# Performance work log

Measured on AMD Instinct MI355X. Metric: run time of the kernel, lower is better.

## Reference

```python
import jax, jax.numpy as jnp
import numpy as np

D = 512
H = 8
DH = D // H  # 64


def setup_inputs() -> dict:
    key = jax.random.key(0)
    ks = jax.random.split(key, 7)
    batch, la, lb = 8, 256, 256
    A = jax.random.normal(ks[0], (batch, la, D), dtype=jnp.float32)
    B = jax.random.normal(ks[1], (batch, lb, D), dtype=jnp.float32)
    s = 1.0 / np.sqrt(D)
    W1 = jax.random.uniform(ks[2], (D, D), minval=-s, maxval=s, dtype=jnp.float32)
    b1 = jax.random.uniform(ks[3], (D,), minval=-s, maxval=s, dtype=jnp.float32)
    W2 = jax.random.uniform(ks[4], (D, D), minval=-s, maxval=s, dtype=jnp.float32)
    b2 = jax.random.uniform(ks[5], (D,), minval=-s, maxval=s, dtype=jnp.float32)
    q = jax.random.normal(ks[6], (DH,), dtype=jnp.float32) * 0.1
    return {"A": A, "B": B, "W1": W1, "b1": b1, "W2": W2, "b2": b2, "q": q}


def reference(A, B, W1, b1, W2, b2, q):
    bs, la, _ = A.shape
    lb = B.shape[1]
    # Linear + ReLU, then raw row-major reshape to (batch, heads, len, dh)
    # (matches torch .view semantics: NOT a head-transpose split)
    A_ = jax.nn.relu(A @ W1.T + b1).reshape(bs, H, la, DH)
    B_ = jax.nn.relu(B @ W2.T + b2).reshape(bs, H, lb, DH)
    # bilinear score: tanh of elementwise pairwise product, dotted with q
    # att_maps: [bs, H, la, lb]
    att_maps = jnp.einsum(
        "bhijc,c->bhij",
        jnp.tanh(A_[:, :, :, None, :] * B_[:, :, None, :, :]),
        q,
    )
    temp_b2a = jax.nn.softmax(jnp.mean(att_maps, axis=3), axis=2)  # [bs,H,la]
    temp_a2b = jax.nn.softmax(jnp.mean(att_maps, axis=2), axis=2)  # [bs,H,lb]
    A_heads = A.reshape(bs, H, la, DH)
    B_heads = B.reshape(bs, H, lb, DH)
    A_p = jnp.sum(A_heads * temp_b2a[..., None], axis=2).reshape(bs, -1)  # [bs, d]
    B_p = jnp.sum(B_heads * temp_a2b[..., None], axis=2).reshape(bs, -1)  # [bs, d]
    return (
        jnp.concatenate((A_p, B_p), axis=1),
        jnp.mean(temp_b2a, axis=1),
        jnp.mean(temp_a2b, axis=1),
    )
```

## Files before the change

kernel.cpp:

```cpp
#include <hip/hip_runtime.h>
#include <hip/hip_bf16.h>

#define LOG2E 1.4426950408889634f
#define SC2   2.8853900817779268f

typedef __attribute__((ext_vector_type(8))) short short8b;
typedef __attribute__((ext_vector_type(4))) short short4b;
typedef __attribute__((ext_vector_type(4))) float f32x4;

__device__ __forceinline__ float fast_exp2(float x) {
#if __has_builtin(__builtin_amdgcn_exp2f)
  return __builtin_amdgcn_exp2f(x);
#else
  return exp2f(x);
#endif
}
__device__ __forceinline__ float fast_rcp(float x) {
#if __has_builtin(__builtin_amdgcn_rcpf)
  return __builtin_amdgcn_rcpf(x);
#else
  return 1.0f / x;
#endif
}
__device__ __forceinline__ short f2bf(float f) {
  __hip_bfloat16 h = __float2bfloat16(f);
  return *reinterpret_cast<short*>(&h);
}

__global__ __launch_bounds__(256) void gemm_fused_kernel(
    const float* __restrict__ Xa, const float* __restrict__ Wa,
    const float* __restrict__ ba, float* __restrict__ Oa,
    const float* __restrict__ Xb, const float* __restrict__ Wb,
    const float* __restrict__ bb, const float* __restrict__ q,
    float2* __restrict__ Cb, unsigned* __restrict__ Cnt,
    float* __restrict__ Ksum) {
  const int isB = blockIdx.z;
  const float* X = isB ? Xb : Xa;
  const float* W = isB ? Wb : Wa;
  const float* bias = isB ? bb : ba;

  __shared__ __align__(16) short As[64 * 40];
  __shared__ __align__(16) short Ws[64 * 40];
  __shared__ __align__(16) float Btile[64][65];
  __shared__ float qls[64];

  int t = threadIdx.x;
  int m0 = blockIdx.x * 64, n0 = blockIdx.y * 64;
  int l = t & 63, w = t >> 6;
  int wm = (w >> 1) * 32, wn = (w & 1) * 32;
  int lr = l & 15, ko = (l >> 4) * 8;

  if (isB && t < 64) qls[t] = q[t];

  f32x4 acc[2][2];
#pragma unroll
  for (int m = 0; m < 2; ++m)
#pragma unroll
    for (int n = 0; n < 2; ++n) acc[m][n] = f32x4{0.f, 0.f, 0.f, 0.f};

  for (int k0 = 0; k0 < 512; k0 += 32) {
#pragma unroll
    for (int s = 0; s < 2; ++s) {
      int slot = t + s * 256;
      int row = slot >> 3, qd = (slot & 7) << 2;
      float4 v = *reinterpret_cast<const float4*>(&X[(m0 + row) * 512 + k0 + qd]);
      short4b sv = {f2bf(v.x), f2bf(v.y), f2bf(v.z), f2bf(v.w)};
      *reinterpret_cast<short4b*>(&As[row * 40 + qd]) = sv;
      float4 u = *reinterpret_cast<const float4*>(&W[(n0 + row) * 512 + k0 + qd]);
      short4b su = {f2bf(u.x), f2bf(u.y), f2bf(u.z), f2bf(u.w)};
      *reinterpret_cast<short4b*>(&Ws[row * 40 + qd]) = su;
    }
    __syncthreads();

    short8b afr[2], bfr[2];
#pragma unroll
    for (int m = 0; m < 2; ++m)
      afr[m] = *reinterpret_cast<const short8b*>(&As[(wm + m * 16 + lr) * 40 + ko]);
#pragma unroll
    for (int n = 0; n < 2; ++n)
      bfr[n] = *reinterpret_cast<const short8b*>(&Ws[(wn + n * 16 + lr) * 40 + ko]);
#pragma unroll
    for (int m = 0; m < 2; ++m)
#pragma unroll
      for (int n = 0; n < 2; ++n)
        acc[m][n] = __builtin_amdgcn_mfma_f32_16x16x32_bf16(afr[m], bfr[n], acc[m][n], 0, 0, 0);
    __syncthreads();
  }

  if (!isB) {
#pragma unroll
    for (int n = 0; n < 2; ++n) {
      int col = n0 + wn + n * 16 + lr;
      float bv = bias[col];
#pragma unroll
      for (int m = 0; m < 2; ++m) {
        int rbase = m0 + wm + m * 16 + (l >> 4) * 4;
#pragma unroll
        for (int r = 0; r < 4; ++r) {
          float v = acc[m][n][r] + bv;
          Oa[(rbase + r) * 512 + col] = v > 0.f ? v : 0.f;
        }
      }
    }
    return;
  }

#pragma unroll
  for (int n = 0; n < 2; ++n) {
    int col = wn + n * 16 + lr;
    float bv = bias[n0 + col];
#pragma unroll
    for (int m = 0; m < 2; ++m) {
      int rbase = wm + m * 16 + (l >> 4) * 4;
#pragma unroll
      for (int r = 0; r < 4; ++r) {
        float v = acc[m][n][r] + bv;
        Btile[rbase + r][col] = v > 0.f ? v : 0.f;
      }
    }
  }
  __syncthreads();

  int jl = t >> 2, p = t & 3;
  int row = m0 + jl;
  int bh = (row >> 8) * 8 + ((row >> 5) & 7);
  int j = ((row & 31) << 3) + (n0 >> 6);
  int c0 = p * 16;

  int nz = 0;
  float K = 0.f;
#pragma unroll
  for (int cc = 0; cc < 16; ++cc) {
    float v = Btile[jl][c0 + cc];
    if (v > 0.f) { ++nz; K += qls[c0 + cc]; }
  }
  int incl = nz;
#pragma unroll
  for (int d = 1; d < 4; d <<= 1) {
    int u = __shfl_up(incl, d, 4);
    if (p >= d) incl += u;
  }
  int off = incl - nz;
  int total = __shfl(incl, 3, 4);

  float2* dst = Cb + (bh * 256 + j) * 64;
  int k = off;
#pragma unroll
  for (int cc = 0; cc < 16; ++cc) {
    int c = c0 + cc;
    float v = Btile[jl][c];
    if (v > 0.f) {
      unsigned qb = (__float_as_uint(-2.f * qls[c]) & ~63u) | (unsigned)c;
      dst[k] = make_float2(v * SC2, __uint_as_float(qb));
      ++k;
    }
  }
  K += __shfl_xor(K, 1, 4);
  K += __shfl_xor(K, 2, 4);
  if (p == 3) {
    int cnt = total;
    while (cnt & 3) { dst[cnt] = make_float2(0.f, 0.f); ++cnt; }
    Cnt[bh * 256 + j] = (unsigned)cnt;
    Ksum[bh * 256 + j] = K;
  }
}

__global__ __launch_bounds__(512, 8) void attmap_kernel(
    const float* __restrict__ Ar, const float2* __restrict__ Cb,
    const unsigned* __restrict__ Cnt,
    float* __restrict__ rowpart, float* __restrict__ colsum) {
  int bh = blockIdx.x, jblk = blockIdx.y, isplit = blockIdx.z;
  int t = threadIdx.x;
  int il = t & 127;
  int g = __builtin_amdgcn_readfirstlane(t >> 7);
  __shared__ __align__(16) float Als[128 * 65];
  __shared__ float red[512];
  __shared__ float cpart[8][8];

  const float* Abase = Ar + bh * 16384 + isplit * 8192;
#pragma unroll
  for (int it = 0; it < 4; ++it) {
    int idx = it * 512 + t;
    int r = idx >> 4, c4 = (idx & 15) << 2;
    float4 v = *reinterpret_cast<const float4*>(&Abase[r * 64 + c4]);
    Als[r * 65 + c4 + 0] = v.x; Als[r * 65 + c4 + 1] = v.y;
    Als[r * 65 + c4 + 2] = v.z; Als[r * 65 + c4 + 3] = v.w;
  }
  __syncthreads();

  const float* Arow = &Als[il * 65];
  float acc[8];

#pragma unroll
  for (int jj = 0; jj < 8; ++jj) {
    int jl = g * 8 + jj;
    int n = (int)__builtin_amdgcn_readfirstlane(Cnt[bh * 256 + jblk * 32 + jl]);
    const float4* P4 = reinterpret_cast<const float4*>(Cb + (bh * 256 + jblk * 32 + jl) * 64);
    float s0 = 0.f, s1 = 0.f;
    if (n > 0) {
      const int nit = n >> 2;
      float4 u0 = P4[0], v0 = P4[1];
      int i1 = (1 < nit) ? 1 : (nit - 1);
      float4 u1 = P4[i1 * 2], v1 = P4[i1 * 2 + 1];
#pragma unroll 1
      for (int it = 0; it < nit; ++it) {
        int i2 = it + 2; i2 = (i2 < nit) ? i2 : (nit - 1);
        float4 u2 = P4[i2 * 2], v2 = P4[i2 * 2 + 1];
        float g0 = Arow[__float_as_uint(u0.y) & 63u];
        float g1 = Arow[__float_as_uint(u0.w) & 63u];
        float g2 = Arow[__float_as_uint(v0.y) & 63u];
        float g3 = Arow[__float_as_uint(v0.w) & 63u];
        float e0 = fast_exp2(g0 * u0.x);
        float e1 = fast_exp2(g1 * u0.z);
        float e2 = fast_exp2(g2 * v0.x);
        float e3 = fast_exp2(g3 * v0.z);
        float w0 = e0 + 1.f, w1 = e1 + 1.f, w2 = e2 + 1.f, w3 = e3 + 1.f;
        float n01 = fmaf(u0.w, w0, u0.y * w1);
        float n23 = fmaf(v0.w, w2, v0.y * w3);
        s0 = fmaf(n01, fast_rcp(w0 * w1), s0);
        s1 = fmaf(n23, fast_rcp(w2 * w3), s1);
        u0 = u1; v0 = v1; u1 = u2; v1 = v2;
      }
    }
    acc[jj] = s0 + s1;
  }

  float rs = 0.f;
#pragma unroll
  for (int jj = 0; jj < 8; ++jj) rs += acc[jj];
  red[t] = rs;

  int lane = t & 63, w = t >> 6;
#pragma unroll
  for (int jj = 0; jj < 8; ++jj) {
    float v = acc[jj];
#pragma unroll
    for (int off = 32; off >= 1; off >>= 1) v += __shfl_xor(v, off);
    if (lane == 0) cpart[w][jj] = v;
  }
  __syncthreads();
  if (t < 128) {
    rowpart[(bh * 8 + jblk) * 256 + isplit * 128 + t] =
        red[t] + red[t + 128] + red[t + 256] + red[t + 384];
  } else if (t < 160) {
    int jl = t - 128;
    int gg = jl >> 3, jj = jl & 7;
    colsum[(bh * 2 + isplit) * 256 + jblk * 32 + jl] =
        cpart[2 * gg][jj] + cpart[2 * gg + 1][jj];
  }
}

__global__ __launch_bounds__(512) void softmax_pool_kernel(
    const float* __restrict__ rowpart, const float* __restrict__ colsum,
    const float* __restrict__ Ksum,
    const float* __restrict__ A0, const float* __restrict__ B0,
    float* __restrict__ b2a, float* __restrict__ a2b,
    float* __restrict__ poolA, float* __restrict__ poolB) {
  int bh = blockIdx.x, chunk = blockIdx.y;
  int b = bh >> 3, h = bh & 7;
  int t = threadIdx.x;
  int tt = t & 255;
  int lane = t & 63, w = (t >> 6) & 3;
  __shared__ float redA[4], redB[4], redC[4], redD[4];
  __shared__ float tA[256], tB[256];
  __shared__ float pp[8][64];

  float r = 0.f;
#pragma unroll
  for (int jb = 0; jb < 8; ++jb) r += rowpart[(bh * 8 + jb) * 256 + tt];
  r *= (1.f / 256.f);
  float cs = Ksum[bh * 256 + tt] +
             (colsum[(bh * 2 + 0) * 256 + tt] + colsum[(bh * 2 + 1) * 256 + tt]) * (1.f / 256.f);

  float mr = r, mc = cs;
#pragma unroll
  for (int off = 32; off >= 1; off >>= 1) {
    mr = fmaxf(mr, __shfl_xor(mr, off));
    mc = fmaxf(mc, __shfl_xor(mc, off));
  }
  if (lane == 0) { redA[w] = mr; redB[w] = mc; }
  __syncthreads();
  mr = fmaxf(fmaxf(redA[0], redA[1]), fmaxf(redA[2], redA[3]));
  mc = fmaxf(fmaxf(redB[0], redB[1]), fmaxf(redB[2], redB[3]));

  float er = fast_exp2((r - mr) * LOG2E);
  float ec = fast_exp2((cs - mc) * LOG2E);
  float sr = er, sc = ec;
#pragma unroll
  for (int off = 32; off >= 1; off >>= 1) {
    sr += __shfl_xor(sr, off);
    sc += __shfl_xor(sc, off);
  }
  if (lane == 0) { redC[w] = sr; redD[w] = sc; }
  __syncthreads();
  sr = redC[0] + redC[1] + redC[2] + redC[3];
  sc = redD[0] + redD[1] + redD[2] + redD[3];

  float vb2a = er * fast_rcp(sr);
  float va2b = ec * fast_rcp(sc);
  tA[tt] = vb2a; tB[tt] = va2b;
  if (chunk == 0) {
    b2a[bh * 256 + tt] = vb2a;
    a2b[bh * 256 + tt] = va2b;
  }
  __syncthreads();

  int c = t & 63, isub = t >> 6;
  const float* Ab = A0 + b * 131072 + h * 16384;
  const float* Bb = B0 + b * 131072 + h * 16384;
  float pa = 0.f, pb = 0.f;
#pragma unroll
  for (int ii = 0; ii < 8; ++ii) {
    int i = chunk * 64 + isub * 8 + ii;
    pa = fmaf(Ab[i * 64 + c], tA[i], pa);
    pb = fmaf(Bb[i * 64 + c], tB[i], pb);
  }
  pp[isub][c] = pa;
  __syncthreads();
  if (t < 64) {
    float s = 0.f;
#pragma unroll
    for (int k = 0; k < 8; ++k) s += pp[k][t];
    poolA[(bh * 4 + chunk) * 64 + t] = s;
  }
  __syncthreads();
  pp[isub][c] = pb;
  __syncthreads();
  if (t < 64) {
    float s = 0.f;
#pragma unroll
    for (int k = 0; k < 8; ++k) s += pp[k][t];
    poolB[(bh * 4 + chunk) * 64 + t] = s;
  }
}

__global__ __launch_bounds__(256) void final_kernel(
    const float* __restrict__ poolA, const float* __restrict__ poolB,
    const float* __restrict__ b2a, const float* __restrict__ a2b,
    float* __restrict__ out) {
  int b = blockIdx.x, t = threadIdx.x;
  float s1 = 0.f, s2 = 0.f;
#pragma unroll
  for (int h = 0; h < 8; ++h) {
    s1 += b2a[(b * 8 + h) * 256 + t];
    s2 += a2b[(b * 8 + h) * 256 + t];
  }
  out[8192 + b * 256 + t] = s1 * 0.125f;
  out[10240 + b * 256 + t] = s2 * 0.125f;

#pragma unroll
  for (int hh = 0; hh < 2; ++hh) {
    int idx = hh * 256 + t;
    int h = idx >> 6, c = idx & 63;
    int base = ((b * 8 + h) * 4) * 64 + c;
    float sA = poolA[base] + poolA[base + 64] + poolA[base + 128] + poolA[base + 192];
    float sB = poolB[base] + poolB[base + 64] + poolB[base + 128] + poolB[base + 192];
    out[b * 1024 + h * 64 + c] = sA;
    out[b * 1024 + 512 + h * 64 + c] = sB;
  }
}

extern "C" void kernel_launch(void* const* d_in, const int* in_sizes, int n_in,
                              void* d_out, int out_size, void* d_ws, size_t ws_size,
                              hipStream_t stream) {
  const float* A  = (const float*)d_in[0];
  const float* B  = (const float*)d_in[1];
  const float* W1 = (const float*)d_in[2];
  const float* b1 = (const float*)d_in[3];
  const float* W2 = (const float*)d_in[4];
  const float* b2 = (const float*)d_in[5];
  const float* q  = (const float*)d_in[6];
  float* out = (float*)d_out;
  float* ws = (float*)d_ws;

  float*    Ar      = ws;
  float2*   Cb      = (float2*)(ws + 1048576);
  unsigned* Cnt     = (unsigned*)(ws + 3145728);
  float*    Ksum    = ws + 3162112;
  float*    rowpart = ws + 3178496;
  float*    colsum  = ws + 3309568;
  float*    b2a     = ws + 3342336;
  float*    a2b     = ws + 3358720;
  float*    poolA   = ws + 3375104;
  float*    poolB   = ws + 3391488;

  gemm_fused_kernel<<<dim3(32, 8, 2), 256, 0, stream>>>(
      A, W1, b1, Ar, B, W2, b2, q, Cb, Cnt, Ksum);
  attmap_kernel<<<dim3(64, 8, 2), 512, 0, stream>>>(Ar, Cb, Cnt, rowpart, colsum);
  softmax_pool_kernel<<<dim3(64, 4), 512, 0, stream>>>(
      rowpart, colsum, Ksum, A, B, b2a, a2b, poolA, poolB);
  final_kernel<<<8, 256, 0, stream>>>(poolA, poolB, b2a, a2b, out);
}
```

Baseline: 64.45 us.

## Pre-convert GEMM inputs to bf16 and load MFMA fragments directly from global

Adds a separate kernel that converts A, B, W1 and W2 to bf16 in workspace. The GEMM then reads MFMA operand fragments straight from global memory, with no LDS staging and no barriers, in a fully unrolled K loop. This halves the bytes the GEMM reads and removes its shared-memory round trip and syncs. In exchange it adds an extra launch plus a full read and write pass over the inputs, and each tile row is re-read by several waves through cache instead of being shared via LDS.

```diff
diff --git a/kernel.cpp b/kernel.cpp
--- a/kernel.cpp
+++ b/kernel.cpp
@@ -5,7 +5,6 @@
 #define SC2   2.8853900817779268f
 
 typedef __attribute__((ext_vector_type(8))) short short8b;
-typedef __attribute__((ext_vector_type(4))) short short4b;
 typedef __attribute__((ext_vector_type(4))) float f32x4;
 
 __device__ __forceinline__ float fast_exp2(float x) {
@@ -27,20 +26,36 @@
   return *reinterpret_cast<short*>(&h);
 }
 
+__global__ __launch_bounds__(256) void cvt_kernel(
+    const float* __restrict__ A, const float* __restrict__ B,
+    const float* __restrict__ W1, const float* __restrict__ W2,
+    short* __restrict__ Abf, short* __restrict__ Bbf,
+    short* __restrict__ W1bf, short* __restrict__ W2bf) {
+  int gid = blockIdx.x * 256 + threadIdx.x;
+  const float* src; short* dst; int off;
+  if (gid < 131072)      { src = A;  dst = Abf;  off = gid << 3; }
+  else if (gid < 262144) { src = B;  dst = Bbf;  off = (gid - 131072) << 3; }
+  else if (gid < 294912) { src = W1; dst = W1bf; off = (gid - 262144) << 3; }
+  else                   { src = W2; dst = W2bf; off = (gid - 294912) << 3; }
+  float4 v0 = *reinterpret_cast<const float4*>(src + off);
+  float4 v1 = *reinterpret_cast<const float4*>(src + off + 4);
+  short8b s = {f2bf(v0.x), f2bf(v0.y), f2bf(v0.z), f2bf(v0.w),
+               f2bf(v1.x), f2bf(v1.y), f2bf(v1.z), f2bf(v1.w)};
+  *reinterpret_cast<short8b*>(dst + off) = s;
+}
+
 __global__ __launch_bounds__(256) void gemm_fused_kernel(
-    const float* __restrict__ Xa, const float* __restrict__ Wa,
+    const short* __restrict__ Xa, const short* __restrict__ Wa,
     const float* __restrict__ ba, float* __restrict__ Oa,
-    const float* __restrict__ Xb, const float* __restrict__ Wb,
+    const short* __restrict__ Xb, const short* __restrict__ Wb,
     const float* __restrict__ bb, const float* __restrict__ q,
     float2* __restrict__ Cb, unsigned* __restrict__ Cnt,
     float* __restrict__ Ksum) {
   const int isB = blockIdx.z;
-  const float* X = isB ? Xb : Xa;
-  const float* W = isB ? Wb : Wa;
+  const short* X = isB ? Xb : Xa;
+  const short* W = isB ? Wb : Wa;
   const float* bias = isB ? bb : ba;
 
-  __shared__ __align__(16) short As[64 * 40];
-  __shared__ __align__(16) short Ws[64 * 40];
   __shared__ __align__(16) float Btile[64][65];
   __shared__ float qls[64];
 
@@ -58,33 +73,19 @@
 #pragma unroll
     for (int n = 0; n < 2; ++n) acc[m][n] = f32x4{0.f, 0.f, 0.f, 0.f};
 
+  const short* pA = X + (m0 + wm + lr) * 512 + ko;
+  const short* pW = W + (n0 + wn + lr) * 512 + ko;
+
+#pragma unroll
   for (int k0 = 0; k0 < 512; k0 += 32) {
-#pragma unroll
-    for (int s = 0; s < 2; ++s) {
-      int slot = t + s * 256;
-      int row = slot >> 3, qd = (slot & 7) << 2;
-      float4 v = *reinterpret_cast<const float4*>(&X[(m0 + row) * 512 + k0 + qd]);
-      short4b sv = {f2bf(v.x), f2bf(v.y), f2bf(v.z), f2bf(v.w)};
-      *reinterpret_cast<short4b*>(&As[row * 40 + qd]) = sv;
-      float4 u = *reinterpret_cast<const float4*>(&W[(n0 + row) * 512 + k0 + qd]);
-      short4b su = {f2bf(u.x), f2bf(u.y), f2bf(u.z), f2bf(u.w)};
-      *reinterpret_cast<short4b*>(&Ws[row * 40 + qd]) = su;
-    }
-    __syncthreads();
-
-    short8b afr[2], bfr[2];
-#pragma unroll
-    for (int m = 0; m < 2; ++m)
-      afr[m] = *reinterpret_cast<const short8b*>(&As[(wm + m * 16 + lr) * 40 + ko]);
-#pragma unroll
-    for (int n = 0; n < 2; ++n)
-      bfr[n] = *reinterpret_cast<const short8b*>(&Ws[(wn + n * 16 + lr) * 40 + ko]);
-#pragma unroll
-    for (int m = 0; m < 2; ++m)
-#pragma unroll
-      for (int n = 0; n < 2; ++n)
-        acc[m][n] = __builtin_amdgcn_mfma_f32_16x16x32_bf16(afr[m], bfr[n], acc[m][n], 0, 0, 0);
-    __syncthreads();
+    short8b a0 = *reinterpret_cast<const short8b*>(pA + k0);
+    short8b a1 = *reinterpret_cast<const short8b*>(pA + 8192 + k0);
+    short8b b0 = *reinterpret_cast<const short8b*>(pW + k0);
+    short8b b1 = *reinterpret_cast<const short8b*>(pW + 8192 + k0);
+    acc[0][0] = __builtin_amdgcn_mfma_f32_16x16x32_bf16(a0, b0, acc[0][0], 0, 0, 0);
+    acc[0][1] = __builtin_amdgcn_mfma_f32_16x16x32_bf16(a0, b1, acc[0][1], 0, 0, 0);
+    acc[1][0] = __builtin_amdgcn_mfma_f32_16x16x32_bf16(a1, b0, acc[1][0], 0, 0, 0);
+    acc[1][1] = __builtin_amdgcn_mfma_f32_16x16x32_bf16(a1, b1, acc[1][1], 0, 0, 0);
   }
 
   if (!isB) {
@@ -121,7 +122,8 @@
   }
   __syncthreads();
 
-  int jl = t >> 2, p = t & 3;
+  int jl = t >> 2, p = t & 2 ? (t & 3) : (t & 3);
+  p = t & 3;
   int row = m0 + jl;
   int bh = (row >> 8) * 8 + ((row >> 5) & 7);
   int j = ((row & 31) << 3) + (n0 >> 6);
@@ -374,18 +376,23 @@
   float* ws = (float*)d_ws;
 
   float*    Ar      = ws;
-  float2*   Cb      = (float2*)(ws + 1048576);
-  unsigned* Cnt     = (unsigned*)(ws + 3145728);
-  float*    Ksum    = ws + 3162112;
-  float*    rowpart = ws + 3178496;
-  float*    colsum  = ws + 3309568;
-  float*    b2a     = ws + 3342336;
-  float*    a2b     = ws + 3358720;
-  float*    poolA   = ws + 3375104;
-  float*    poolB   = ws + 3391488;
-
+  short*    Abf     = (short*)(ws + 1048576);
+  short*    Bbf     = (short*)(ws + 1572864);
+  short*    W1bf    = (short*)(ws + 2097152);
+  short*    W2bf    = (short*)(ws + 2228224);
+  float2*   Cb      = (float2*)(ws + 2359296);
+  unsigned* Cnt     = (unsigned*)(ws + 4456448);
+  float*    Ksum    = ws + 4472832;
+  float*    rowpart = ws + 4489216;
+  float*    colsum  = ws + 4620288;
+  float*    b2a     = ws + 4653056;
+  float*    a2b     = ws + 4669440;
+  float*    poolA   = ws + 4685824;
+  float*    poolB   = ws + 4702208;
+
+  cvt_kernel<<<1280, 256, 0, stream>>>(A, B, W1, W2, Abf, Bbf, W1bf, W2bf);
   gemm_fused_kernel<<<dim3(32, 8, 2), 256, 0, stream>>>(
-      A, W1, b1, Ar, B, W2, b2, q, Cb, Cnt, Ksum);
+      Abf, W1bf, b1, Ar, Bbf, W2bf, b2, q, Cb, Cnt, Ksum);
   attmap_kernel<<<dim3(64, 8, 2), 512, 0, stream>>>(Ar, Cb, Cnt, rowpart, colsum);
   softmax_pool_kernel<<<dim3(64, 4), 512, 0, stream>>>(
       rowpart, colsum, Ksum, A, B, b2a, a2b, poolA, poolB);
```

Measured after the change: 74.33 us. +15.3%, slower.

## Fuse softmax-pool and final reduction kernels into one launch

Applied to the files above, without the earlier changes.

Merges the softmax/pooling kernel and the final head-averaging kernel into a single kernel with one block per (batch, head). Each block now pools over all 256 rows itself and writes pooled outputs directly, and the head-0 block recomputes the softmaxes of all 8 heads to produce the head-averaged attention vectors. This removes a kernel launch and the intermediate workspace round trip, at the cost of fewer blocks (64 instead of 256) and serialized redundant softmax work in the h==0 blocks, which lengthens the critical path.

```diff
diff --git a/kernel.cpp b/kernel.cpp
--- a/kernel.cpp
+++ b/kernel.cpp
@@ -250,13 +250,12 @@
   }
 }
 
-__global__ __launch_bounds__(512) void softmax_pool_kernel(
+__global__ __launch_bounds__(512) void softmax_final_kernel(
     const float* __restrict__ rowpart, const float* __restrict__ colsum,
     const float* __restrict__ Ksum,
     const float* __restrict__ A0, const float* __restrict__ B0,
-    float* __restrict__ b2a, float* __restrict__ a2b,
-    float* __restrict__ poolA, float* __restrict__ poolB) {
-  int bh = blockIdx.x, chunk = blockIdx.y;
+    float* __restrict__ out) {
+  int bh = blockIdx.x;
   int b = bh >> 3, h = bh & 7;
   int t = threadIdx.x;
   int tt = t & 255;
@@ -265,98 +264,117 @@
   __shared__ float tA[256], tB[256];
   __shared__ float pp[8][64];
 
-  float r = 0.f;
-#pragma unroll
-  for (int jb = 0; jb < 8; ++jb) r += rowpart[(bh * 8 + jb) * 256 + tt];
-  r *= (1.f / 256.f);
-  float cs = Ksum[bh * 256 + tt] +
-             (colsum[(bh * 2 + 0) * 256 + tt] + colsum[(bh * 2 + 1) * 256 + tt]) * (1.f / 256.f);
-
-  float mr = r, mc = cs;
-#pragma unroll
-  for (int off = 32; off >= 1; off >>= 1) {
-    mr = fmaxf(mr, __shfl_xor(mr, off));
-    mc = fmaxf(mc, __shfl_xor(mc, off));
-  }
-  if (lane == 0) { redA[w] = mr; redB[w] = mc; }
+  {
+    float r = 0.f;
+#pragma unroll
+    for (int jb = 0; jb < 8; ++jb) r += rowpart[(bh * 8 + jb) * 256 + tt];
+    r *= (1.f / 256.f);
+    float cs = Ksum[bh * 256 + tt] +
+               (colsum[(bh * 2 + 0) * 256 + tt] + colsum[(bh * 2 + 1) * 256 + tt]) * (1.f / 256.f);
+
+    float mr = r, mc = cs;
+#pragma unroll
+    for (int off = 32; off >= 1; off >>= 1) {
+      mr = fmaxf(mr, __shfl_xor(mr, off));
+      mc = fmaxf(mc, __shfl_xor(mc, off));
+    }
+    if (lane == 0) { redA[w] = mr; redB[w] = mc; }
+    __syncthreads();
+    mr = fmaxf(fmaxf(redA[0], redA[1]), fmaxf(redA[2], redA[3]));
+    mc = fmaxf(fmaxf(redB[0], redB[1]), fmaxf(redB[2], redB[3]));
+
+    float er = fast_exp2((r - mr) * LOG2E);
+    float ec = fast_exp2((cs - mc) * LOG2E);
+    float sr = er, sc = ec;
+#pragma unroll
+    for (int off = 32; off >= 1; off >>= 1) {
+      sr += __shfl_xor(sr, off);
+      sc += __shfl_xor(sc, off);
+    }
+    if (lane == 0) { redC[w] = sr; redD[w] = sc; }
+    __syncthreads();
+    sr = redC[0] + redC[1] + redC[2] + redC[3];
+    sc = redD[0] + redD[1] + redD[2] + redD[3];
+
+    tA[tt] = er * fast_rcp(sr);
+    tB[tt] = ec * fast_rcp(sc);
+  }
   __syncthreads();
-  mr = fmaxf(fmaxf(redA[0], redA[1]), fmaxf(redA[2], redA[3]));
-  mc = fmaxf(fmaxf(redB[0], redB[1]), fmaxf(redB[2], redB[3]));
-
-  float er = fast_exp2((r - mr) * LOG2E);
-  float ec = fast_exp2((cs - mc) * LOG2E);
-  float sr = er, sc = ec;
-#pragma unroll
-  for (int off = 32; off >= 1; off >>= 1) {
-    sr += __shfl_xor(sr, off);
-    sc += __shfl_xor(sc, off);
-  }
-  if (lane == 0) { redC[w] = sr; redD[w] = sc; }
-  __syncthreads();
-  sr = redC[0] + redC[1] + redC[2] + redC[3];
-  sc = redD[0] + redD[1] + redD[2] + redD[3];
-
-  float vb2a = er * fast_rcp(sr);
-  float va2b = ec * fast_rcp(sc);
-  tA[tt] = vb2a; tB[tt] = va2b;
-  if (chunk == 0) {
-    b2a[bh * 256 + tt] = vb2a;
-    a2b[bh * 256 + tt] = va2b;
-  }
-  __syncthreads();
-
-  int c = t & 63, isub = t >> 6;
-  const float* Ab = A0 + b * 131072 + h * 16384;
-  const float* Bb = B0 + b * 131072 + h * 16384;
-  float pa = 0.f, pb = 0.f;
-#pragma unroll
-  for (int ii = 0; ii < 8; ++ii) {
-    int i = chunk * 64 + isub * 8 + ii;
-    pa = fmaf(Ab[i * 64 + c], tA[i], pa);
-    pb = fmaf(Bb[i * 64 + c], tB[i], pb);
-  }
-  pp[isub][c] = pa;
-  __syncthreads();
-  if (t < 64) {
-    float s = 0.f;
-#pragma unroll
-    for (int k = 0; k < 8; ++k) s += pp[k][t];
-    poolA[(bh * 4 + chunk) * 64 + t] = s;
-  }
-  __syncthreads();
-  pp[isub][c] = pb;
-  __syncthreads();
-  if (t < 64) {
-    float s = 0.f;
-#pragma unroll
-    for (int k = 0; k < 8; ++k) s += pp[k][t];
-    poolB[(bh * 4 + chunk) * 64 + t] = s;
-  }
-}
-
-__global__ __launch_bounds__(256) void final_kernel(
-    const float* __restrict__ poolA, const float* __restrict__ poolB,
-    const float* __restrict__ b2a, const float* __restrict__ a2b,
-    float* __restrict__ out) {
-  int b = blockIdx.x, t = threadIdx.x;
-  float s1 = 0.f, s2 = 0.f;
-#pragma unroll
-  for (int h = 0; h < 8; ++h) {
-    s1 += b2a[(b * 8 + h) * 256 + t];
-    s2 += a2b[(b * 8 + h) * 256 + t];
-  }
-  out[8192 + b * 256 + t] = s1 * 0.125f;
-  out[10240 + b * 256 + t] = s2 * 0.125f;
-
-#pragma unroll
-  for (int hh = 0; hh < 2; ++hh) {
-    int idx = hh * 256 + t;
-    int h = idx >> 6, c = idx & 63;
-    int base = ((b * 8 + h) * 4) * 64 + c;
-    float sA = poolA[base] + poolA[base + 64] + poolA[base + 128] + poolA[base + 192];
-    float sB = poolB[base] + poolB[base + 64] + poolB[base + 128] + poolB[base + 192];
-    out[b * 1024 + h * 64 + c] = sA;
-    out[b * 1024 + 512 + h * 64 + c] = sB;
+
+  {
+    int c = t & 63, iq = t >> 6;
+    const float* Ab = A0 + b * 131072 + h * 16384;
+    const float* Bb = B0 + b * 131072 + h * 16384;
+    float pa = 0.f, pb = 0.f;
+#pragma unroll 4
+    for (int ii = 0; ii < 32; ++ii) {
+      int i = (iq << 5) + ii;
+      pa = fmaf(Ab[i * 64 + c], tA[i], pa);
+      pb = fmaf(Bb[i * 64 + c], tB[i], pb);
+    }
+    pp[iq][c] = pa;
+    __syncthreads();
+    if (t < 64) {
+      float s = 0.f;
+#pragma unroll
+      for (int k = 0; k < 8; ++k) s += pp[k][t];
+      out[b * 1024 + h * 64 + t] = s;
+    }
+    __syncthreads();
+    pp[iq][c] = pb;
+    __syncthreads();
+    if (t < 64) {
+      float s = 0.f;
+#pragma unroll
+      for (int k = 0; k < 8; ++k) s += pp[k][t];
+      out[b * 1024 + 512 + h * 64 + t] = s;
+    }
+  }
+
+  if (h == 0) {
+    float mRacc = 0.f, mCacc = 0.f;
+#pragma unroll 1
+    for (int hp = 0; hp < 8; ++hp) {
+      int bhp = b * 8 + hp;
+      float r = 0.f;
+#pragma unroll
+      for (int jb = 0; jb < 8; ++jb) r += rowpart[(bhp * 8 + jb) * 256 + tt];
+      r *= (1.f / 256.f);
+      float cs = Ksum[bhp * 256 + tt] +
+                 (colsum[(bhp * 2 + 0) * 256 + tt] + colsum[(bhp * 2 + 1) * 256 + tt]) * (1.f / 256.f);
+
+      float mr = r, mc = cs;
+#pragma unroll
+      for (int off = 32; off >= 1; off >>= 1) {
+        mr = fmaxf(mr, __shfl_xor(mr, off));
+        mc = fmaxf(mc, __shfl_xor(mc, off));
+      }
+      __syncthreads();
+      if (lane == 0) { redA[w] = mr; redB[w] = mc; }
+      __syncthreads();
+      mr = fmaxf(fmaxf(redA[0], redA[1]), fmaxf(redA[2], redA[3]));
+      mc = fmaxf(fmaxf(redB[0], redB[1]), fmaxf(redB[2], redB[3]));
+
+      float er = fast_exp2((r - mr) * LOG2E);
+      float ec = fast_exp2((cs - mc) * LOG2E);
+      float sr = er, sc = ec;
+#pragma unroll
+      for (int off = 32; off >= 1; off >>= 1) {
+        sr += __shfl_xor(sr, off);
+        sc += __shfl_xor(sc, off);
+      }
+      if (lane == 0) { redC[w] = sr; redD[w] = sc; }
+      __syncthreads();
+      sr = redC[0] + redC[1] + redC[2] + redC[3];
+      sc = redD[0] + redD[1] + redD[2] + redD[3];
+
+      mRacc += er * fast_rcp(sr);
+      mCacc += ec * fast_rcp(sc);
+    }
+    if (t < 256) {
+      out[8192 + b * 256 + t] = mRacc * 0.125f;
+      out[10240 + b * 256 + t] = mCacc * 0.125f;
+    }
   }
 }
 
@@ -379,15 +397,10 @@
   float*    Ksum    = ws + 3162112;
   float*    rowpart = ws + 3178496;
   float*    colsum  = ws + 3309568;
-  float*    b2a     = ws + 3342336;
-  float*    a2b     = ws + 3358720;
-  float*    poolA   = ws + 3375104;
-  float*    poolB   = ws + 3391488;
 
   gemm_fused_kernel<<<dim3(32, 8, 2), 256, 0, stream>>>(
       A, W1, b1, Ar, B, W2, b2, q, Cb, Cnt, Ksum);
   attmap_kernel<<<dim3(64, 8, 2), 512, 0, stream>>>(Ar, Cb, Cnt, rowpart, colsum);
-  softmax_pool_kernel<<<dim3(64, 4), 512, 0, stream>>>(
-      rowpart, colsum, Ksum, A, B, b2a, a2b, poolA, poolB);
-  final_kernel<<<8, 256, 0, stream>>>(poolA, poolB, b2a, a2b, out);
-}
+  softmax_final_kernel<<<64, 512, 0, stream>>>(
+      rowpart, colsum, Ksum, A, B, out);
+}
```

Result: slower. 74.86 us (+16.2%).
